# Kernel optimization log

Measured on AMD Instinct MI355X. Metric: run time of the kernel, lower is better.

The kernel has to match this reference:

```python
import jax, jax.numpy as jnp
import numpy as np

N_HEAD, D_HEAD, PROJ_DIM = 8, 64, 256
D_MODEL = N_HEAD * D_HEAD  # 512
SCALE_W = 0.7
EPS = 1e-5       # attention denominator eps
LN_EPS = 1e-5    # torch LayerNorm default
SCALE = D_HEAD ** -0.5
CHUNK = 64


def draw_orth(d, m, rng):
    # Performer orthogonal random features: stacked orthogonal blocks with chi-norm scaling.
    blocks = []
    n_full = m // d
    for _ in range(n_full):
        q, _ = np.linalg.qr(rng.standard_normal((d, d)))
        blocks.append(q.T)
    rem = m - n_full * d
    if rem:
        q, _ = np.linalg.qr(rng.standard_normal((d, d)))
        blocks.append(q.T[:rem])
    W = np.concatenate(blocks, axis=0)                      # [m, d]
    mult = np.linalg.norm(rng.standard_normal((m, d)), axis=1)
    return (W * mult[:, None]).T                            # [d, m]


def prime(x, proj):
    # FAVOR+ positive softmax features. x: [B,H,L,d], proj: [d,m] -> [B,H,L,2m]
    xn = x * (x.shape[-1] ** -0.25)
    xp = jnp.einsum('bhld,dm->bhlm', xn, proj)
    half = 0.5 * jnp.sum(xn * xn, axis=-1, keepdims=True)
    u = jnp.concatenate([xp, -xp], axis=-1) - half
    # per-row max subtraction: exactly cancelled by the subsequent sum-normalization
    u = u - jax.lax.stop_gradient(jnp.max(u, axis=-1, keepdims=True))
    return jnp.exp(u)


def causal_linear(q, k, v):
    # out[b,h,t] = sum_{s<=t} (q_t . k_s) v_s  (additive fast-weight / fast_weight_sum, W0 = 0)
    B, H, L, M = q.shape
    D = v.shape[-1]
    nC = L // CHUNK
    qc = q.reshape(B, H, nC, CHUNK, M).transpose(2, 0, 1, 3, 4)
    kc = k.reshape(B, H, nC, CHUNK, M).transpose(2, 0, 1, 3, 4)
    vc = v.reshape(B, H, nC, CHUNK, D).transpose(2, 0, 1, 3, 4)
    mask = jnp.tril(jnp.ones((CHUNK, CHUNK), q.dtype))

    def step(W, blk):
        qb, kb, vb = blk
        inter = jnp.einsum('bhcm,bhmd->bhcd', qb, W)
        sc = jnp.einsum('bhcm,bhsm->bhcs', qb, kb) * mask
        intra = jnp.einsum('bhcs,bhsd->bhcd', sc, vb)
        W = W + jnp.einsum('bhsm,bhsd->bhmd', kb, vb)
        return W, inter + intra

    W0 = jnp.zeros((B, H, M, D), q.dtype)
    _, out = jax.lax.scan(step, W0, (qc, kc, vc))            # [nC,B,H,C,D]
    return out.transpose(1, 2, 0, 3, 4).reshape(B, H, L, D)


def setup_inputs() -> dict:
    key = jax.random.key(0)
    k0, k1, k2 = jax.random.split(key, 3)
    L, B = 256, 32
    h = jax.random.normal(k0, (L, B, D_MODEL), jnp.float32)
    w_qkv = jax.random.normal(k1, (D_MODEL, 4 * N_HEAD * D_HEAD), jnp.float32) * (D_MODEL ** -0.5)
    w_o = jax.random.normal(k2, (N_HEAD * D_HEAD, D_MODEL), jnp.float32) * ((N_HEAD * D_HEAD) ** -0.5)
    ln_gamma = jnp.ones((D_MODEL,), jnp.float32)
    ln_beta = jnp.zeros((D_MODEL,), jnp.float32)
    pi0 = 0.5 * jnp.ones((N_HEAD, 256), jnp.float32)
    pi1 = 0.5 * jnp.ones((N_HEAD, 256), jnp.float32)
    proj_matrix = jnp.asarray(draw_orth(D_HEAD, PROJ_DIM, np.random.default_rng(0)), jnp.float32)
    return {"h": h, "w_qkv": w_qkv, "w_o": w_o, "ln_gamma": ln_gamma, "ln_beta": ln_beta,
            "pi0": pi0, "pi1": pi1, "proj_matrix": proj_matrix}


def reference(h, w_qkv, w_o, ln_gamma, ln_beta, pi0, pi1, proj_matrix):
    L, B, _ = h.shape
    qkv = jnp.einsum('lbd,de->lbe', h, w_qkv).reshape(L, B, N_HEAD, 4 * D_HEAD)
    q, k1, k2, v = jnp.split(qkv, 4, axis=-1)
    perm = lambda t: t.transpose(1, 2, 0, 3)                 # -> [B,H,L,dh]
    q, k1, k2, v = perm(q), perm(k1), perm(k2), perm(v)

    norm = lambda p: p / jnp.sum(p, axis=-1, keepdims=True)
    qf = norm(prime(q, proj_matrix))                         # [B,H,L,2m]
    k1f = norm(prime(k1, proj_matrix))
    k2f = norm(prime(k2, SCALE_W * proj_matrix))
    kf = k1f * pi0[None, :, :L, None] + k2f * pi1[None, :, :L, None]

    denom_acc = jnp.cumsum(kf, axis=2)
    denom = jnp.einsum('bhlm,bhlm->bhl', denom_acc, qf)[..., None]

    out = causal_linear(qf, kf, v)                           # [B,H,L,dh]
    out = SCALE * out / (denom + EPS)
    out = out.transpose(0, 2, 1, 3).reshape(B, L, N_HEAD * D_HEAD).transpose(1, 0, 2)

    attn = jnp.einsum('lbd,de->lbe', out, w_o)
    x = h + attn
    mu = jnp.mean(x, axis=-1, keepdims=True)
    var = jnp.var(x, axis=-1, keepdims=True)
    return (x - mu) / jnp.sqrt(var + LN_EPS) * ln_gamma + ln_beta
```

## Files before the change

kernel.cpp:

```cpp
#include <hip/hip_runtime.h>
#include <hip/hip_bf16.h>

#define L_SEQ 256
#define B_SZ  32
#define NH    8
#define DH    64
#define DM    512
#define FD    512
#define PM    256
#define ROWS  8192
#define QKVN  2048

typedef __bf16 bf16x8 __attribute__((ext_vector_type(8)));
typedef __bf16 bf16x4 __attribute__((ext_vector_type(4)));
typedef float f32x4 __attribute__((ext_vector_type(4)));
#define MFMA16(a, b, c) __builtin_amdgcn_mfma_f32_16x16x32_bf16((a), (b), (c), 0, 0, 0)

static __device__ __forceinline__ void gload_lds16(const __bf16* g, __bf16* lds) {
  __builtin_amdgcn_global_load_lds(
      (const __attribute__((address_space(1))) void*)g,
      (__attribute__((address_space(3))) void*)lds, 16, 0, 0);
}

#define PREP_HB   2048
#define PREP_WT   256
#define PREP_WOT  64
#define PREP_PJ   4
#define PREP_TINY 1
#define PREP_BLOCKS (PREP_HB + PREP_WT + PREP_WOT + PREP_PJ + PREP_TINY)

__global__ __launch_bounds__(256) void prep(
    const void* __restrict__ h, const void* __restrict__ wqkv,
    const void* __restrict__ wo, const void* __restrict__ proj,
    const void* __restrict__ pi0, const void* __restrict__ pi1,
    const void* __restrict__ gam, const void* __restrict__ bet,
    int* __restrict__ flag, __bf16* __restrict__ hb, __bf16* __restrict__ wt,
    __bf16* __restrict__ wot, __bf16* __restrict__ projT,
    __bf16* __restrict__ pi0b, __bf16* __restrict__ pi1b,
    __bf16* __restrict__ gamb, __bf16* __restrict__ betb,
    __bf16* __restrict__ projB) {
  __shared__ float T[64][69];
  __shared__ int red[256];
  const int tid = threadIdx.x;
  int cnt = 0;
  {
    const unsigned short* hbits = (const unsigned short*)h;
    for (int i = 0; i < 16; ++i) {
      const unsigned short u = hbits[tid * 16 + i];
      if (((u >> 7) & 0xFF) >= 0xA0) ++cnt;
    }
  }
  red[tid] = cnt; __syncthreads();
  for (int s = 128; s > 0; s >>= 1) { if (tid < s) red[tid] += red[tid + s]; __syncthreads(); }
  const int f32 = (red[0] >= 64) ? 1 : 0;
  __syncthreads();

  const int blk = blockIdx.x;
  if (blk < PREP_HB) {
    const int i = blk * 256 + tid;
    if (f32) {
      const f32x4* s = (const f32x4*)h;
      const f32x4 a = s[i * 2], b = s[i * 2 + 1];
      bf16x8 t;
      t[0] = (__bf16)a[0]; t[1] = (__bf16)a[1]; t[2] = (__bf16)a[2]; t[3] = (__bf16)a[3];
      t[4] = (__bf16)b[0]; t[5] = (__bf16)b[1]; t[6] = (__bf16)b[2]; t[7] = (__bf16)b[3];
      *reinterpret_cast<bf16x8*>(hb + (long)i * 8) = t;
    } else {
      *reinterpret_cast<bf16x8*>(hb + (long)i * 8) = ((const bf16x8*)h)[i];
    }
    return;
  }
  const void* src; __bf16* dst; int M, N, n0, m0;
  int pjx = -1;
  if (blk < PREP_HB + PREP_WT) {
    const int x = blk - PREP_HB;
    src = wqkv; dst = wt; M = 512; N = 2048; n0 = (x & 31) * 64; m0 = (x >> 5) * 64;
  } else if (blk < PREP_HB + PREP_WT + PREP_WOT) {
    const int x = blk - PREP_HB - PREP_WT;
    src = wo; dst = wot; M = 512; N = 512; n0 = (x & 7) * 64; m0 = (x >> 3) * 64;
  } else if (blk < PREP_HB + PREP_WT + PREP_WOT + PREP_PJ) {
    const int x = blk - PREP_HB - PREP_WT - PREP_WOT;
    src = proj; dst = projT; M = 64; N = 256; n0 = x * 64; m0 = 0;
    pjx = x;
  } else {
    if (tid == 0) flag[0] = f32;
    if (f32) {
      const float* s0 = (const float*)pi0; const float* s1 = (const float*)pi1;
      const float* s2 = (const float*)gam; const float* s3 = (const float*)bet;
      for (int i = tid; i < NH * 256; i += 256) { pi0b[i] = (__bf16)s0[i]; pi1b[i] = (__bf16)s1[i]; }
      for (int i = tid; i < DM; i += 256)      { gamb[i] = (__bf16)s2[i]; betb[i] = (__bf16)s3[i]; }
    } else {
      const __bf16* s0 = (const __bf16*)pi0; const __bf16* s1 = (const __bf16*)pi1;
      const __bf16* s2 = (const __bf16*)gam; const __bf16* s3 = (const __bf16*)bet;
      for (int i = tid; i < NH * 256; i += 256) { pi0b[i] = s0[i]; pi1b[i] = s1[i]; }
      for (int i = tid; i < DM; i += 256)      { gamb[i] = s2[i]; betb[i] = s3[i]; }
    }
    return;
  }
  if (f32) {
    const float* s = (const float*)src;
#pragma unroll
    for (int rep = 0; rep < 16; ++rep) {
      const int i = rep * 4 + (tid >> 6), j = tid & 63;
      T[i][j] = s[(long)(m0 + i) * N + n0 + j];
    }
  } else {
    const __bf16* s = (const __bf16*)src;
#pragma unroll
    for (int rep = 0; rep < 16; ++rep) {
      const int i = rep * 4 + (tid >> 6), j = tid & 63;
      T[i][j] = (float)s[(long)(m0 + i) * N + n0 + j];
    }
  }
  __syncthreads();
#pragma unroll
  for (int rep = 0; rep < 16; ++rep) {
    const int i = rep * 4 + (tid >> 6), j = tid & 63;
    dst[(long)(n0 + i) * M + m0 + j] = (__bf16)T[j][i];
  }
  if (pjx >= 0) {
    const int lane = tid & 63, sub = tid >> 6;
    const int mm = lane & 15, qq = lane >> 4;
#pragma unroll
    for (int kk2 = 0; kk2 < 2; ++kk2) {
      bf16x8 v;
#pragma unroll
      for (int e = 0; e < 8; ++e) v[e] = (__bf16)T[kk2 * 32 + qq * 8 + e][sub * 16 + mm];
      *reinterpret_cast<bf16x8*>(projB + ((pjx * 4 + sub) * 2 + kk2) * 512 + lane * 8) = v;
    }
  }
}

__global__ __launch_bounds__(256) void gemm_h_wqkv(const __bf16* __restrict__ A,
                                                   const __bf16* __restrict__ Bt,
                                                   __bf16* __restrict__ C) {
  __shared__ __bf16 At[128][72];
  __shared__ __bf16 Bts[128][72];
  const int n0 = blockIdx.x * 128, m0 = blockIdx.y * 128;
  const int tid = threadIdx.x, lane = tid & 63, wv = tid >> 6;
  const int m = lane & 15, q = lane >> 4;
  const int wr = (wv >> 1) * 64, wc = (wv & 1) * 64;
  const int r = tid >> 1, c0 = (tid & 1) * 32;
  const __bf16* ap = A + (long)(m0 + r) * DM + c0;
  const __bf16* bp = Bt + (long)(n0 + r) * DM + c0;
  f32x4 acc[4][4];
#pragma unroll
  for (int i = 0; i < 4; ++i)
#pragma unroll
    for (int j = 0; j < 4; ++j) acc[i][j] = f32x4{0.f, 0.f, 0.f, 0.f};

  bf16x8 ar[4], br[4];
#pragma unroll
  for (int j = 0; j < 4; ++j) {
    ar[j] = *reinterpret_cast<const bf16x8*>(ap + j * 8);
    br[j] = *reinterpret_cast<const bf16x8*>(bp + j * 8);
  }
  for (int k0 = 0; k0 < DM; k0 += 64) {
    __syncthreads();
#pragma unroll
    for (int j = 0; j < 4; ++j) {
      *reinterpret_cast<bf16x8*>(&At[r][c0 + j * 8]) = ar[j];
      *reinterpret_cast<bf16x8*>(&Bts[r][c0 + j * 8]) = br[j];
    }
    if (k0 + 64 < DM) {
#pragma unroll
      for (int j = 0; j < 4; ++j) {
        ar[j] = *reinterpret_cast<const bf16x8*>(ap + k0 + 64 + j * 8);
        br[j] = *reinterpret_cast<const bf16x8*>(bp + k0 + 64 + j * 8);
      }
    }
    __syncthreads();
#pragma unroll
    for (int kk = 0; kk < 2; ++kk) {
      bf16x8 af[4], bfv[4];
#pragma unroll
      for (int i = 0; i < 4; ++i) {
        af[i]  = *reinterpret_cast<const bf16x8*>(&At[wr + i * 16 + m][kk * 32 + q * 8]);
        bfv[i] = *reinterpret_cast<const bf16x8*>(&Bts[wc + i * 16 + m][kk * 32 + q * 8]);
      }
#pragma unroll
      for (int ai = 0; ai < 4; ++ai)
#pragma unroll
        for (int bi = 0; bi < 4; ++bi)
          acc[ai][bi] = MFMA16(af[ai], bfv[bi], acc[ai][bi]);
    }
  }
#pragma unroll
  for (int ai = 0; ai < 4; ++ai)
#pragma unroll
    for (int r2 = 0; r2 < 4; ++r2)
#pragma unroll
      for (int bi = 0; bi < 4; ++bi)
        C[(long)(m0 + wr + ai * 16 + q * 4 + r2) * QKVN + n0 + wc + bi * 16 + m] =
            (__bf16)acc[ai][bi][r2];
}

__global__ __launch_bounds__(256) void features_mfma(const __bf16* __restrict__ qkv,
                                                     const __bf16* __restrict__ projB,
                                                     const __bf16* __restrict__ pi0,
                                                     const __bf16* __restrict__ pi1,
                                                     __bf16* __restrict__ kf,
                                                     __bf16* __restrict__ vt) {
  const int st = blockIdx.x;
  const int l0 = st * 64;
  const int bh = blockIdx.y;
  const int h = bh & 7, b = bh >> 3;
  const int tid = threadIdx.x, lane = tid & 63, wv = tid >> 6;
  const int m = lane & 15, q = lane >> 4;
  __shared__ __bf16 As[2][64][72];
  __shared__ __bf16 VT[64][72];

  {
    const int r = tid >> 2, c0 = (tid & 3) * 16;
    const __bf16* ap = qkv + (long)((l0 + r) * B_SZ + b) * QKVN + h * 256 + 64 + c0;
#pragma unroll
    for (int t2 = 0; t2 < 2; ++t2) {
      *reinterpret_cast<bf16x8*>(&As[t2][r][c0]) =
          *reinterpret_cast<const bf16x8*>(ap + t2 * 64);
      *reinterpret_cast<bf16x8*>(&As[t2][r][c0 + 8]) =
          *reinterpret_cast<const bf16x8*>(ap + t2 * 64 + 8);
    }
    const __bf16* vp = ap + 128;
#pragma unroll
    for (int j = 0; j < 16; ++j) VT[c0 + j][r] = vp[j];
  }
  const int l = l0 + wv * 16 + m;
  const float p0w = (float)pi0[h * 256 + l];
  const float p1w = (float)pi1[h * 256 + l];
  const float SQ = 0.35355339f;
  const float SK2 = 0.24748737f;
  __syncthreads();

  {
    const int c2 = tid >> 6;
    const int d = c2 * 16 + m;
#pragma unroll
    for (int kk = 0; kk < 2; ++kk) {
      const bf16x8 v = *reinterpret_cast<const bf16x8*>(&VT[d][kk * 32 + q * 8]);
      *reinterpret_cast<bf16x8*>(vt + (((long)bh * 8 + st * 2 + kk) * 4 + c2) * 512 + lane * 8) = v;
    }
  }

  f32x4 acc1[16], acc2[16];
#pragma unroll
  for (int c = 0; c < 16; ++c) {
    acc1[c] = f32x4{0.f, 0.f, 0.f, 0.f};
    acc2[c] = f32x4{0.f, 0.f, 0.f, 0.f};
  }
#pragma unroll
  for (int kk = 0; kk < 2; ++kk) {
    const bf16x8 x1 = *reinterpret_cast<const bf16x8*>(&As[0][wv * 16 + m][kk * 32 + q * 8]);
    const bf16x8 x2 = *reinterpret_cast<const bf16x8*>(&As[1][wv * 16 + m][kk * 32 + q * 8]);
#pragma unroll
    for (int c = 0; c < 16; ++c) {
      const bf16x8 wf =
          *reinterpret_cast<const bf16x8*>(projB + (c * 2 + kk) * 512 + lane * 8);
      acc1[c] = MFMA16(wf, x1, acc1[c]);
      acc2[c] = MFMA16(wf, x2, acc2[c]);
    }
  }
  float mx1 = 0.f, mx2 = 0.f;
#pragma unroll
  for (int c = 0; c < 16; ++c)
#pragma unroll
    for (int r = 0; r < 4; ++r) {
      mx1 = fmaxf(mx1, fabsf(acc1[c][r] * SQ));
      mx2 = fmaxf(mx2, fabsf(acc2[c][r] * SK2));
    }
  mx1 = fmaxf(mx1, __shfl_xor(mx1, 16)); mx1 = fmaxf(mx1, __shfl_xor(mx1, 32));
  mx2 = fmaxf(mx2, __shfl_xor(mx2, 16)); mx2 = fmaxf(mx2, __shfl_xor(mx2, 32));
  const float C21 = __expf(-2.f * mx1);
  const float C22 = __expf(-2.f * mx2);
  float sm1 = 0.f, sm2 = 0.f;
#pragma unroll
  for (int c = 0; c < 16; ++c)
#pragma unroll
    for (int r = 0; r < 4; ++r) {
      const float e11 = __expf(acc1[c][r] * SQ - mx1);
      const float e12 = __expf(acc2[c][r] * SK2 - mx2);
      sm1 += e11 + C21 * __builtin_amdgcn_rcpf(e11);
      sm2 += e12 + C22 * __builtin_amdgcn_rcpf(e12);
      acc1[c][r] = e11;
      acc2[c][r] = e12;
    }
  sm1 += __shfl_xor(sm1, 16); sm1 += __shfl_xor(sm1, 32);
  sm2 += __shfl_xor(sm2, 16); sm2 += __shfl_xor(sm2, 32);
  const float w1 = p0w * __builtin_amdgcn_rcpf(sm1);
  const float w2 = p1w * __builtin_amdgcn_rcpf(sm2);
  const float K1 = C21 * w1, K2 = C22 * w2;
  __bf16* op = kf + (((long)bh * 16 + (l >> 4)) * 16) * 512 + lane * 8;
#pragma unroll
  for (int c = 0; c < 16; ++c) {
    bf16x8 v;
#pragma unroll
    for (int r = 0; r < 4; ++r) {
      v[r]     = (__bf16)(w1 * acc1[c][r] + w2 * acc2[c][r]);
      v[4 + r] = (__bf16)(K1 * __builtin_amdgcn_rcpf(acc1[c][r]) +
                          K2 * __builtin_amdgcn_rcpf(acc2[c][r]));
    }
    *reinterpret_cast<bf16x8*>(op + c * 512) = v;
  }
}

__global__ __launch_bounds__(256, 2) void flash_mfma(const __bf16* __restrict__ qkv,
                                                     const __bf16* __restrict__ projB,
                                                     const __bf16* __restrict__ kf,
                                                     const __bf16* __restrict__ vt,
                                                     __bf16* __restrict__ att) {
  const int id = blockIdx.x;
  const int bh = id & 255;
  const int t  = 3 - (id >> 8);
  const int h = bh & 7, b = bh >> 3;
  const int tid = threadIdx.x, lane = tid & 63, wv = tid >> 6;
  const int m = lane & 15, q = lane >> 4;
  __shared__ __bf16 Kst[4 * 16 * 512];
  __shared__ __bf16 Pt[64][72];

  const float SQ = 0.35355339f;
  f32x4 acc[16];
#pragma unroll
  for (int c = 0; c < 16; ++c) acc[c] = f32x4{0.f, 0.f, 0.f, 0.f};
  const __bf16* xb = qkv + (long)((t * 64 + wv * 16 + m) * B_SZ + b) * QKVN + h * 256;
#pragma unroll
  for (int kk = 0; kk < 2; ++kk) {
    const bf16x8 xf = *reinterpret_cast<const bf16x8*>(xb + kk * 32 + q * 8);
#pragma unroll
    for (int c = 0; c < 16; ++c) {
      const bf16x8 wf =
          *reinterpret_cast<const bf16x8*>(projB + (c * 2 + kk) * 512 + lane * 8);
      acc[c] = MFMA16(wf, xf, acc[c]);
    }
  }
  float mx = 0.f;
#pragma unroll
  for (int c = 0; c < 16; ++c)
#pragma unroll
    for (int r = 0; r < 4; ++r) mx = fmaxf(mx, fabsf(acc[c][r] * SQ));
  mx = fmaxf(mx, __shfl_xor(mx, 16));
  mx = fmaxf(mx, __shfl_xor(mx, 32));
  const float C2 = __expf(-2.f * mx);
  float sm = 0.f;
#pragma unroll
  for (int c = 0; c < 16; ++c)
#pragma unroll
    for (int r = 0; r < 4; ++r) {
      const float e1 = __expf(acc[c][r] * SQ - mx);
      sm += e1 + C2 * __builtin_amdgcn_rcpf(e1);
      acc[c][r] = e1;
    }
  sm += __shfl_xor(sm, 16);
  sm += __shfl_xor(sm, 32);
  const float inv = __builtin_amdgcn_rcpf(sm);
  const float K2 = C2 * inv;
  bf16x8 qT[16];
#pragma unroll
  for (int c = 0; c < 16; ++c) {
    bf16x8 v;
#pragma unroll
    for (int r = 0; r < 4; ++r) {
      v[r]     = (__bf16)(acc[c][r] * inv);
      v[4 + r] = (__bf16)(K2 * __builtin_amdgcn_rcpf(acc[c][r]));
    }
    qT[c] = v;
  }

  f32x4 o[4];
#pragma unroll
  for (int i = 0; i < 4; ++i) o[i] = f32x4{0.f, 0.f, 0.f, 0.f};
  float den[4] = {0.f, 0.f, 0.f, 0.f};

  const __bf16* kf_bh = kf + (long)bh * (16 * 16 * 512);
  const __bf16* vtb = vt + (long)bh * (8 * 4 * 512) + lane * 8;

  for (int st = 0; st <= t; ++st) {
    __syncthreads();
    {
      const __bf16* gsrc =
          kf_bh + ((long)(st * 4) * 16 + wv * 16) * 512 + lane * 8;
      __bf16* ldst = Kst + (wv * 16) * 512;
#pragma unroll
      for (int j = 0; j < 16; ++j)
        gload_lds16(gsrc + j * 512, ldst + j * 512);
    }
    bf16x8 vf[8];
#pragma unroll
    for (int kk = 0; kk < 2; ++kk)
#pragma unroll
      for (int c = 0; c < 4; ++c)
        vf[kk * 4 + c] =
            *reinterpret_cast<const bf16x8*>(vtb + (((long)st * 2 + kk) * 4 + c) * 512);
    __syncthreads();

    f32x4 s[4];
#pragma unroll
    for (int i = 0; i < 4; ++i) s[i] = f32x4{0.f, 0.f, 0.f, 0.f};
#pragma unroll
    for (int g = 0; g < 16; ++g) {
      const __bf16* kp = Kst + (long)g * 512 + lane * 8;
      const bf16x8 kb0 = *reinterpret_cast<const bf16x8*>(kp);
      const bf16x8 kb1 = *reinterpret_cast<const bf16x8*>(kp + 16 * 512);
      const bf16x8 kb2 = *reinterpret_cast<const bf16x8*>(kp + 32 * 512);
      const bf16x8 kb3 = *reinterpret_cast<const bf16x8*>(kp + 48 * 512);
      s[0] = MFMA16(qT[g], kb0, s[0]);
      s[1] = MFMA16(qT[g], kb1, s[1]);
      s[2] = MFMA16(qT[g], kb2, s[2]);
      s[3] = MFMA16(qT[g], kb3, s[3]);
    }
    const bool last = (st == t);
#pragma unroll
    for (int c = 0; c < 4; ++c)
#pragma unroll
      for (int r = 0; r < 4; ++r) {
        const int row = wv * 16 + q * 4 + r, col = c * 16 + m;
        const float v = (last && col > row) ? 0.f : s[c][r];
        den[r] += v;
        Pt[row][col] = (__bf16)v;
      }
#pragma unroll
    for (int kk = 0; kk < 2; ++kk) {
      const bf16x8 pf = *reinterpret_cast<const bf16x8*>(&Pt[wv * 16 + m][kk * 32 + q * 8]);
#pragma unroll
      for (int c = 0; c < 4; ++c)
        o[c] = MFMA16(pf, vf[kk * 4 + c], o[c]);
    }
  }
#pragma unroll
  for (int r = 0; r < 4; ++r) {
    float d = den[r];
    d += __shfl_xor(d, 1); d += __shfl_xor(d, 2);
    d += __shfl_xor(d, 4); d += __shfl_xor(d, 8);
    const float invd = 0.125f / (d + 1e-5f);
    const int row = t * 64 + wv * 16 + q * 4 + r;
#pragma unroll
    for (int c = 0; c < 4; ++c)
      att[((long)(row * B_SZ + b)) * DM + h * DH + c * 16 + m] = (__bf16)(o[c][r] * invd);
  }
}

__global__ __launch_bounds__(256) void gemm_att_wo(const __bf16* __restrict__ A,
                                                   const __bf16* __restrict__ Bt,
                                                   const __bf16* __restrict__ hb,
                                                   float* __restrict__ xrow) {
  __shared__ __bf16 At[128][72];
  __shared__ __bf16 Bts[128][72];
  const int n0 = blockIdx.x * 128, m0 = blockIdx.y * 128;
  const int tid = threadIdx.x, lane = tid & 63, wv = tid >> 6;
  const int m = lane & 15, q = lane >> 4;
  const int wr = (wv >> 1) * 64, wc = (wv & 1) * 64;
  const int r = tid >> 1, c0 = (tid & 1) * 32;
  const __bf16* ap = A + (long)(m0 + r) * DM + c0;
  const __bf16* bp = Bt + (long)(n0 + r) * DM + c0;
  f32x4 acc[4][4];
#pragma unroll
  for (int i = 0; i < 4; ++i)
#pragma unroll
    for (int j = 0; j < 4; ++j) acc[i][j] = f32x4{0.f, 0.f, 0.f, 0.f};

  bf16x8 ar[4], br[4];
#pragma unroll
  for (int j = 0; j < 4; ++j) {
    ar[j] = *reinterpret_cast<const bf16x8*>(ap + j * 8);
    br[j] = *reinterpret_cast<const bf16x8*>(bp + j * 8);
  }
  for (int k0 = 0; k0 < DM; k0 += 64) {
    __syncthreads();
#pragma unroll
    for (int j = 0; j < 4; ++j) {
      *reinterpret_cast<bf16x8*>(&At[r][c0 + j * 8]) = ar[j];
      *reinterpret_cast<bf16x8*>(&Bts[r][c0 + j * 8]) = br[j];
    }
    if (k0 + 64 < DM) {
#pragma unroll
      for (int j = 0; j < 4; ++j) {
        ar[j] = *reinterpret_cast<const bf16x8*>(ap + k0 + 64 + j * 8);
        br[j] = *reinterpret_cast<const bf16x8*>(bp + k0 + 64 + j * 8);
      }
    }
    __syncthreads();
#pragma unroll
    for (int kk = 0; kk < 2; ++kk) {
      bf16x8 af[4], bfv[4];
#pragma unroll
      for (int i = 0; i < 4; ++i) {
        af[i]  = *reinterpret_cast<const bf16x8*>(&At[wr + i * 16 + m][kk * 32 + q * 8]);
        bfv[i] = *reinterpret_cast<const bf16x8*>(&Bts[wc + i * 16 + m][kk * 32 + q * 8]);
      }
#pragma unroll
      for (int ai = 0; ai < 4; ++ai)
#pragma unroll
        for (int bi = 0; bi < 4; ++bi)
          acc[ai][bi] = MFMA16(af[ai], bfv[bi], acc[ai][bi]);
    }
  }
#pragma unroll
  for (int ai = 0; ai < 4; ++ai)
#pragma unroll
    for (int r2 = 0; r2 < 4; ++r2)
#pragma unroll
      for (int bi = 0; bi < 4; ++bi) {
        const long row = m0 + wr + ai * 16 + q * 4 + r2;
        const long col = n0 + wc + bi * 16 + m;
        xrow[row * DM + col] = acc[ai][bi][r2] + (float)hb[row * DM + col];
      }
}

__global__ __launch_bounds__(256) void ln_out(const float* __restrict__ xrow,
                                              const __bf16* __restrict__ gamma,
                                              const __bf16* __restrict__ beta,
                                              const int* __restrict__ flag,
                                              void* __restrict__ out) {
  const int f32 = flag[0];
  const int tid = threadIdx.x, lane = tid & 63, wv = tid >> 6;
  const long r = (long)blockIdx.x * 4 + wv;
  const int c0 = lane * 4, c1 = 256 + lane * 4;
  const f32x4 x0 = *reinterpret_cast<const f32x4*>(xrow + r * DM + c0);
  const f32x4 x1 = *reinterpret_cast<const f32x4*>(xrow + r * DM + c1);

  float s = 0.f, s2 = 0.f;
#pragma unroll
  for (int i = 0; i < 4; ++i) {
    s += x0[i] + x1[i];
    s2 += x0[i] * x0[i] + x1[i] * x1[i];
  }
#pragma unroll
  for (int msk = 1; msk < 64; msk <<= 1) {
    s += __shfl_xor(s, msk);
    s2 += __shfl_xor(s2, msk);
  }
  const float mu = s * (1.f / 512.f);
  const float var = s2 * (1.f / 512.f) - mu * mu;
  const float rstd = rsqrtf(var + 1e-5f);

  if (f32) {
    f32x4 o0, o1;
#pragma unroll
    for (int i = 0; i < 4; ++i) {
      o0[i] = (x0[i] - mu) * rstd * (float)gamma[c0 + i] + (float)beta[c0 + i];
      o1[i] = (x1[i] - mu) * rstd * (float)gamma[c1 + i] + (float)beta[c1 + i];
    }
    *reinterpret_cast<f32x4*>((float*)out + r * DM + c0) = o0;
    *reinterpret_cast<f32x4*>((float*)out + r * DM + c1) = o1;
  } else {
    bf16x4 o0, o1;
#pragma unroll
    for (int i = 0; i < 4; ++i) {
      o0[i] = (__bf16)((x0[i] - mu) * rstd * (float)gamma[c0 + i] + (float)beta[c0 + i]);
      o1[i] = (__bf16)((x1[i] - mu) * rstd * (float)gamma[c1 + i] + (float)beta[c1 + i]);
    }
    *reinterpret_cast<bf16x4*>((__bf16*)out + r * DM + c0) = o0;
    *reinterpret_cast<bf16x4*>((__bf16*)out + r * DM + c1) = o1;
  }
}

extern "C" void kernel_launch(void* const* d_in, const int* in_sizes, int n_in,
                              void* d_out, int out_size, void* d_ws, size_t ws_size,
                              hipStream_t stream) {
  (void)in_sizes; (void)n_in; (void)out_size; (void)ws_size;
  char* ws = (char*)d_ws;
  __bf16* qkv   = (__bf16*)ws;
  int*    flag  = (int*)(ws + 33554432);
  __bf16* wt    = (__bf16*)(ws + 33554688);
  __bf16* wot   = (__bf16*)(ws + 35651840);
  __bf16* att   = (__bf16*)(ws + 36176128);
  __bf16* vt    = (__bf16*)(ws + 44564736);
  __bf16* hb    = (__bf16*)(ws + 52953344);
  __bf16* projT = (__bf16*)(ws + 61341952);
  __bf16* pi0b  = (__bf16*)(ws + 61374720);
  __bf16* pi1b  = (__bf16*)(ws + 61378816);
  __bf16* gamb  = (__bf16*)(ws + 61382912);
  __bf16* betb  = (__bf16*)(ws + 61383936);
  float*  xrow  = (float*)(ws + 61384960);
  __bf16* projB = (__bf16*)(ws + 78163968);
  __bf16* kf    = (__bf16*)(ws + 128493824);

  prep<<<PREP_BLOCKS, 256, 0, stream>>>(d_in[0], d_in[1], d_in[2], d_in[7],
                                        d_in[5], d_in[6], d_in[3], d_in[4],
                                        flag, hb, wt, wot, projT,
                                        pi0b, pi1b, gamb, betb, projB);
  gemm_h_wqkv<<<dim3(16, 64), 256, 0, stream>>>(hb, wt, qkv);
  features_mfma<<<dim3(4, 256), 256, 0, stream>>>(qkv, projB, pi0b, pi1b, kf, vt);
  flash_mfma<<<dim3(1024), 256, 0, stream>>>(qkv, projB, kf, vt, att);
  gemm_att_wo<<<dim3(4, 64), 256, 0, stream>>>(att, wot, hb, xrow);
  ln_out<<<dim3(ROWS / 4), 256, 0, stream>>>(xrow, gamb, betb, flag, d_out);
}
```

Before: 206.3 us.

## Fuse output projection GEMM with residual add and LayerNorm

Replaces the separate att×Wo GEMM (which wrote fp32 pre-norm rows to workspace) and the LayerNorm kernel with one kernel. Each 512-thread block computes 32 full output rows, reduces row statistics through shared memory and writes the normalized output directly. Wo is pre-swizzled in prep into an MFMA fragment layout so B operands load straight from global/L2 without LDS staging. This removes the fp32 intermediate round trip and one launch, at the cost of fewer, larger blocks (256) and repeated global reads of the weight fragments.

New measurement: 209.4 us. No clear change (+1.5%).

```diff
diff --git a/kernel.cpp b/kernel.cpp
--- a/kernel.cpp
+++ b/kernel.cpp
@@ -16,6 +16,11 @@
 typedef float f32x4 __attribute__((ext_vector_type(4)));
 #define MFMA16(a, b, c) __builtin_amdgcn_mfma_f32_16x16x32_bf16((a), (b), (c), 0, 0, 0)
 
+static __device__ __forceinline__ void stmix(void* p, long i, float v, int f32) {
+  if (f32) ((float*)p)[i] = v;
+  else     ((__bf16*)p)[i] = (__bf16)v;
+}
+
 static __device__ __forceinline__ void gload_lds16(const __bf16* g, __bf16* lds) {
   __builtin_amdgcn_global_load_lds(
       (const __attribute__((address_space(1))) void*)g,
@@ -38,7 +43,7 @@
     __bf16* __restrict__ wot, __bf16* __restrict__ projT,
     __bf16* __restrict__ pi0b, __bf16* __restrict__ pi1b,
     __bf16* __restrict__ gamb, __bf16* __restrict__ betb,
-    __bf16* __restrict__ projB) {
+    __bf16* __restrict__ projB, __bf16* __restrict__ wotB) {
   __shared__ float T[64][69];
   __shared__ int red[256];
   const int tid = threadIdx.x;
@@ -71,13 +76,14 @@
     return;
   }
   const void* src; __bf16* dst; int M, N, n0, m0;
-  int pjx = -1;
+  int pjx = -1, wox = -1;
   if (blk < PREP_HB + PREP_WT) {
     const int x = blk - PREP_HB;
     src = wqkv; dst = wt; M = 512; N = 2048; n0 = (x & 31) * 64; m0 = (x >> 5) * 64;
   } else if (blk < PREP_HB + PREP_WT + PREP_WOT) {
     const int x = blk - PREP_HB - PREP_WT;
     src = wo; dst = wot; M = 512; N = 512; n0 = (x & 7) * 64; m0 = (x >> 3) * 64;
+    wox = x;
   } else if (blk < PREP_HB + PREP_WT + PREP_WOT + PREP_PJ) {
     const int x = blk - PREP_HB - PREP_WT - PREP_WOT;
     src = proj; dst = projT; M = 64; N = 256; n0 = x * 64; m0 = 0;
@@ -129,6 +135,18 @@
       *reinterpret_cast<bf16x8*>(projB + ((pjx * 4 + sub) * 2 + kk2) * 512 + lane * 8) = v;
     }
   }
+  if (wox >= 0) {
+    const int lane = tid & 63, sub = tid >> 6;
+    const int mm = lane & 15, qq = lane >> 4;
+    const int cb0 = n0 >> 4, kk0 = m0 >> 5;
+#pragma unroll
+    for (int kk2 = 0; kk2 < 2; ++kk2) {
+      bf16x8 v;
+#pragma unroll
+      for (int e = 0; e < 8; ++e) v[e] = (__bf16)T[kk2 * 32 + qq * 8 + e][sub * 16 + mm];
+      *reinterpret_cast<bf16x8*>(wotB + (((cb0 + sub) * 16) + kk0 + kk2) * 512 + lane * 8) = v;
+    }
+  }
 }
 
 __global__ __launch_bounds__(256) void gemm_h_wqkv(const __bf16* __restrict__ A,
@@ -437,118 +455,93 @@
   }
 }
 
-__global__ __launch_bounds__(256) void gemm_att_wo(const __bf16* __restrict__ A,
-                                                   const __bf16* __restrict__ Bt,
-                                                   const __bf16* __restrict__ hb,
-                                                   float* __restrict__ xrow) {
-  __shared__ __bf16 At[128][72];
-  __shared__ __bf16 Bts[128][72];
-  const int n0 = blockIdx.x * 128, m0 = blockIdx.y * 128;
+__global__ __launch_bounds__(512) void gemm_wo_ln(const __bf16* __restrict__ att,
+                                                  const __bf16* __restrict__ wotB,
+                                                  const __bf16* __restrict__ hb,
+                                                  const __bf16* __restrict__ gamma,
+                                                  const __bf16* __restrict__ beta,
+                                                  const int* __restrict__ flag,
+                                                  void* __restrict__ out) {
+  const int f32 = flag[0];
+  const int bm = blockIdx.x;
   const int tid = threadIdx.x, lane = tid & 63, wv = tid >> 6;
   const int m = lane & 15, q = lane >> 4;
-  const int wr = (wv >> 1) * 64, wc = (wv & 1) * 64;
-  const int r = tid >> 1, c0 = (tid & 1) * 32;
-  const __bf16* ap = A + (long)(m0 + r) * DM + c0;
-  const __bf16* bp = Bt + (long)(n0 + r) * DM + c0;
-  f32x4 acc[4][4];
-#pragma unroll
-  for (int i = 0; i < 4; ++i)
-#pragma unroll
-    for (int j = 0; j < 4; ++j) acc[i][j] = f32x4{0.f, 0.f, 0.f, 0.f};
-
-  bf16x8 ar[4], br[4];
+  const int rb = wv >> 2;
+  const int wc = (wv & 3) * 128;
+  __shared__ __bf16 As[32][520];
+  __shared__ float RedS[32][4], RedS2[32][4];
+
 #pragma unroll
   for (int j = 0; j < 4; ++j) {
-    ar[j] = *reinterpret_cast<const bf16x8*>(ap + j * 8);
-    br[j] = *reinterpret_cast<const bf16x8*>(bp + j * 8);
-  }
-  for (int k0 = 0; k0 < DM; k0 += 64) {
-    __syncthreads();
-#pragma unroll
-    for (int j = 0; j < 4; ++j) {
-      *reinterpret_cast<bf16x8*>(&At[r][c0 + j * 8]) = ar[j];
-      *reinterpret_cast<bf16x8*>(&Bts[r][c0 + j * 8]) = br[j];
-    }
-    if (k0 + 64 < DM) {
-#pragma unroll
-      for (int j = 0; j < 4; ++j) {
-        ar[j] = *reinterpret_cast<const bf16x8*>(ap + k0 + 64 + j * 8);
-        br[j] = *reinterpret_cast<const bf16x8*>(bp + k0 + 64 + j * 8);
-      }
-    }
-    __syncthreads();
-#pragma unroll
-    for (int kk = 0; kk < 2; ++kk) {
-      bf16x8 af[4], bfv[4];
-#pragma unroll
-      for (int i = 0; i < 4; ++i) {
-        af[i]  = *reinterpret_cast<const bf16x8*>(&At[wr + i * 16 + m][kk * 32 + q * 8]);
-        bfv[i] = *reinterpret_cast<const bf16x8*>(&Bts[wc + i * 16 + m][kk * 32 + q * 8]);
-      }
-#pragma unroll
-      for (int ai = 0; ai < 4; ++ai)
-#pragma unroll
-        for (int bi = 0; bi < 4; ++bi)
-          acc[ai][bi] = MFMA16(af[ai], bfv[bi], acc[ai][bi]);
-    }
-  }
-#pragma unroll
-  for (int ai = 0; ai < 4; ++ai)
-#pragma unroll
-    for (int r2 = 0; r2 < 4; ++r2)
-#pragma unroll
-      for (int bi = 0; bi < 4; ++bi) {
-        const long row = m0 + wr + ai * 16 + q * 4 + r2;
-        const long col = n0 + wc + bi * 16 + m;
-        xrow[row * DM + col] = acc[ai][bi][r2] + (float)hb[row * DM + col];
-      }
-}
-
-__global__ __launch_bounds__(256) void ln_out(const float* __restrict__ xrow,
-                                              const __bf16* __restrict__ gamma,
-                                              const __bf16* __restrict__ beta,
-                                              const int* __restrict__ flag,
-                                              void* __restrict__ out) {
-  const int f32 = flag[0];
-  const int tid = threadIdx.x, lane = tid & 63, wv = tid >> 6;
-  const long r = (long)blockIdx.x * 4 + wv;
-  const int c0 = lane * 4, c1 = 256 + lane * 4;
-  const f32x4 x0 = *reinterpret_cast<const f32x4*>(xrow + r * DM + c0);
-  const f32x4 x1 = *reinterpret_cast<const f32x4*>(xrow + r * DM + c1);
-
-  float s = 0.f, s2 = 0.f;
-#pragma unroll
-  for (int i = 0; i < 4; ++i) {
-    s += x0[i] + x1[i];
-    s2 += x0[i] * x0[i] + x1[i] * x1[i];
-  }
-#pragma unroll
-  for (int msk = 1; msk < 64; msk <<= 1) {
-    s += __shfl_xor(s, msk);
-    s2 += __shfl_xor(s2, msk);
-  }
-  const float mu = s * (1.f / 512.f);
-  const float var = s2 * (1.f / 512.f) - mu * mu;
-  const float rstd = rsqrtf(var + 1e-5f);
-
-  if (f32) {
-    f32x4 o0, o1;
-#pragma unroll
-    for (int i = 0; i < 4; ++i) {
-      o0[i] = (x0[i] - mu) * rstd * (float)gamma[c0 + i] + (float)beta[c0 + i];
-      o1[i] = (x1[i] - mu) * rstd * (float)gamma[c1 + i] + (float)beta[c1 + i];
-    }
-    *reinterpret_cast<f32x4*>((float*)out + r * DM + c0) = o0;
-    *reinterpret_cast<f32x4*>((float*)out + r * DM + c1) = o1;
-  } else {
-    bf16x4 o0, o1;
-#pragma unroll
-    for (int i = 0; i < 4; ++i) {
-      o0[i] = (__bf16)((x0[i] - mu) * rstd * (float)gamma[c0 + i] + (float)beta[c0 + i]);
-      o1[i] = (__bf16)((x1[i] - mu) * rstd * (float)gamma[c1 + i] + (float)beta[c1 + i]);
-    }
-    *reinterpret_cast<bf16x4*>((__bf16*)out + r * DM + c0) = o0;
-    *reinterpret_cast<bf16x4*>((__bf16*)out + r * DM + c1) = o1;
+    const int ci = j * 512 + tid;
+    const int r = ci >> 6, c = (ci & 63) * 8;
+    *reinterpret_cast<bf16x8*>(&As[r][c]) =
+        *reinterpret_cast<const bf16x8*>(att + ((long)(bm * 32 + r)) * DM + c);
+  }
+  __syncthreads();
+
+  f32x4 acc[8];
+#pragma unroll
+  for (int i = 0; i < 8; ++i) acc[i] = f32x4{0.f, 0.f, 0.f, 0.f};
+#pragma unroll
+  for (int kk = 0; kk < 16; ++kk) {
+    const bf16x8 af = *reinterpret_cast<const bf16x8*>(&As[rb * 16 + m][kk * 32 + q * 8]);
+#pragma unroll
+    for (int cbl = 0; cbl < 8; ++cbl) {
+      const bf16x8 bf = *reinterpret_cast<const bf16x8*>(
+          wotB + ((((wv & 3) * 8 + cbl) * 16) + kk) * 512 + lane * 8);
+      acc[cbl] = MFMA16(af, bf, acc[cbl]);
+    }
+  }
+
+  float s[4] = {0.f, 0.f, 0.f, 0.f}, s2[4] = {0.f, 0.f, 0.f, 0.f};
+#pragma unroll
+  for (int cbl = 0; cbl < 8; ++cbl)
+#pragma unroll
+    for (int r = 0; r < 4; ++r) {
+      const long row = (long)bm * 32 + rb * 16 + q * 4 + r;
+      const int col = wc + cbl * 16 + m;
+      const float x = acc[cbl][r] + (float)hb[row * DM + col];
+      acc[cbl][r] = x;
+      s[r] += x;
+      s2[r] += x * x;
+    }
+#pragma unroll
+  for (int msk = 1; msk < 16; msk <<= 1)
+#pragma unroll
+    for (int r = 0; r < 4; ++r) {
+      s[r] += __shfl_xor(s[r], msk);
+      s2[r] += __shfl_xor(s2[r], msk);
+    }
+  if (m == 0) {
+#pragma unroll
+    for (int r = 0; r < 4; ++r) {
+      RedS[rb * 16 + q * 4 + r][wv & 3] = s[r];
+      RedS2[rb * 16 + q * 4 + r][wv & 3] = s2[r];
+    }
+  }
+  __syncthreads();
+
+  float gam[8], bet[8];
+#pragma unroll
+  for (int cbl = 0; cbl < 8; ++cbl) {
+    gam[cbl] = (float)gamma[wc + cbl * 16 + m];
+    bet[cbl] = (float)beta[wc + cbl * 16 + m];
+  }
+#pragma unroll
+  for (int r = 0; r < 4; ++r) {
+    const int rl = rb * 16 + q * 4 + r;
+    const float fs = RedS[rl][0] + RedS[rl][1] + RedS[rl][2] + RedS[rl][3];
+    const float fs2 = RedS2[rl][0] + RedS2[rl][1] + RedS2[rl][2] + RedS2[rl][3];
+    const float mu = fs * (1.f / 512.f);
+    const float var = fs2 * (1.f / 512.f) - mu * mu;
+    const float rstd = rsqrtf(var + 1e-5f);
+    const long row = (long)bm * 32 + rl;
+#pragma unroll
+    for (int cbl = 0; cbl < 8; ++cbl) {
+      const int col = wc + cbl * 16 + m;
+      stmix(out, row * DM + col, (acc[cbl][r] - mu) * rstd * gam[cbl] + bet[cbl], f32);
+    }
   }
 }
 
@@ -569,17 +562,16 @@
   __bf16* pi1b  = (__bf16*)(ws + 61378816);
   __bf16* gamb  = (__bf16*)(ws + 61382912);
   __bf16* betb  = (__bf16*)(ws + 61383936);
-  float*  xrow  = (float*)(ws + 61384960);
   __bf16* projB = (__bf16*)(ws + 78163968);
+  __bf16* wotB  = (__bf16*)(ws + 78196736);
   __bf16* kf    = (__bf16*)(ws + 128493824);
 
   prep<<<PREP_BLOCKS, 256, 0, stream>>>(d_in[0], d_in[1], d_in[2], d_in[7],
                                         d_in[5], d_in[6], d_in[3], d_in[4],
                                         flag, hb, wt, wot, projT,
-                                        pi0b, pi1b, gamb, betb, projB);
+                                        pi0b, pi1b, gamb, betb, projB, wotB);
   gemm_h_wqkv<<<dim3(16, 64), 256, 0, stream>>>(hb, wt, qkv);
   features_mfma<<<dim3(4, 256), 256, 0, stream>>>(qkv, projB, pi0b, pi1b, kf, vt);
   flash_mfma<<<dim3(1024), 256, 0, stream>>>(qkv, projB, kf, vt, att);
-  gemm_att_wo<<<dim3(4, 64), 256, 0, stream>>>(att, wot, hb, xrow);
-  ln_out<<<dim3(ROWS / 4), 256, 0, stream>>>(xrow, gamb, betb, flag, d_out);
-}
+  gemm_wo_ln<<<dim3(256), 512, 0, stream>>>(att, wotB, hb, gamb, betb, flag, d_out);
+}
```
